# Kernel optimization log

Hardware: AMD Instinct MI355X
Metric: run time of the kernel (lower is better)

## Reference

```python
import jax, jax.numpy as jnp
import numpy as np


def setup_inputs() -> dict:
    key = jax.random.key(0)
    k1, k2 = jax.random.split(key)
    B, C, H, W = 64, 2048, 16, 16
    P = 200
    x = jax.random.normal(k1, (B, C, H, W), dtype=jnp.float32)
    prototype_vectors = jax.random.normal(k2, (P, C), dtype=jnp.float32)
    return {"x": x, "prototype_vectors": prototype_vectors}


def reference(x, prototype_vectors):
    # x: (B, C, H, W); prototypes: (P, C)
    B, C, H, W = x.shape
    P = prototype_vectors.shape[0]
    x_flat = x.reshape(B, C, H * W)                      # (B, C, S)
    # broadcasted (B,P,C,S) subtraction; same math, GEMM for cross term)
    x_sq = jnp.sum(x_flat * x_flat, axis=1)              # (B, S)
    p_sq = jnp.sum(prototype_vectors * prototype_vectors, axis=1)  # (P,)
    cross = jnp.einsum('pc,bcs->bps', prototype_vectors, x_flat)   # (B, P, S)
    distances = x_sq[:, None, :] + p_sq[None, :, None] - 2.0 * cross  # (B, P, S)
    similarities = -distances
    max_similarities = jnp.max(similarities, axis=2)     # (B, P)
    activation_maps = similarities.reshape(B, P, H, W)   # (B, P, H, W)
    return max_similarities, distances, activation_maps
```

## Files before the change

kernel.cpp:

```cpp
#include <hip/hip_runtime.h>

typedef float floatx4 __attribute__((ext_vector_type(4)));
typedef unsigned short ushortx4 __attribute__((ext_vector_type(4)));
typedef __bf16 bf16x8 __attribute__((ext_vector_type(8)));

#define B_ 64
#define C_ 2048
#define S_ 256
#define P_ 200
#define PM_ 256
#define ST_ 32
#define NST_ 8
#define NKT_ 32

__device__ __forceinline__ unsigned short f2bf(float f) {
  unsigned int u = __float_as_uint(f);
  u += 0x7FFFu + ((u >> 16) & 1u);
  return (unsigned short)(u >> 16);
}

__global__ void __launch_bounds__(256) prep_kernel(const float* __restrict__ proto,
                                                   unsigned short* __restrict__ wsp,
                                                   float* __restrict__ wpsq) {
  const int r = blockIdx.x;
  const int t = threadIdx.x;
  floatx4 v0 = {0.f,0.f,0.f,0.f}, v1 = {0.f,0.f,0.f,0.f};
  if (r < P_) {
    v0 = *reinterpret_cast<const floatx4*>(proto + (size_t)r * C_ + t * 8);
    v1 = *reinterpret_cast<const floatx4*>(proto + (size_t)r * C_ + t * 8 + 4);
  }
  float s = 0.f;
  ushortx4 h0, h1;
#pragma unroll
  for (int i = 0; i < 4; ++i) {
    s += v0[i]*v0[i] + v1[i]*v1[i];
    h0[i] = f2bf(v0[i]); h1[i] = f2bf(v1[i]);
  }
  const int u = (t >> 3) * 16384 + (r >> 4) * 1024 + (t & 7) * 128 + (r & 15) * 8;
  *reinterpret_cast<ushortx4*>(wsp + u) = h0;
  *reinterpret_cast<ushortx4*>(wsp + u + 4) = h1;

#pragma unroll
  for (int o = 32; o > 0; o >>= 1) s += __shfl_down(s, o);
  __shared__ float red[4];
  if ((t & 63) == 0) red[t >> 6] = s;
  __syncthreads();
  if (t == 0) wpsq[r] = red[0] + red[1] + red[2] + red[3];
}

__global__ void __launch_bounds__(512, 4) main_kernel(const float* __restrict__ x,
    const unsigned short* __restrict__ wsp, const float* __restrict__ wpsq,
    float* __restrict__ out_dist, float* __restrict__ out_act,
    float* __restrict__ wpmax) {
  __shared__ unsigned short lds[36864];

  const int t = threadIdx.x;
  const int lane = t & 63;
  const int w = t >> 6;
  const int lg = lane >> 4, l15 = lane & 15;
  const int b = blockIdx.x >> 3, st = blockIdx.x & 7;

  const int s_ = lane & 31;
  const int h_ = lane >> 5;
  const float* xb = x + (size_t)b * (C_ * S_) + (size_t)(w * 8 + h_ * 4) * S_ + st * ST_ + s_;

  const int slot_w = (s_ & 15) ^ ((s_ & 8) >> 1) ^ ((s_ >> 4) << 1);
  const int wr_base = 32768 + (s_ >> 4) * 1024 + w * 128 + slot_w * 8 + h_ * 4;
  const int slot_r0 = l15 ^ ((l15 & 8) >> 1);

  floatx4 acc[2][2] = {};
  float xsq_s = 0.f;

#pragma unroll
  for (int q = 0; q < 4; ++q) {
    __builtin_amdgcn_global_load_lds(
      (const __attribute__((address_space(1))) unsigned int*)(wsp + (q * 512 + t) * 8),
      (__attribute__((address_space(3))) unsigned int*)
        ((__attribute__((address_space(3))) unsigned short*)lds + (q * 512 + t) * 8),
      16, 0, 0);
  }
  {
    float xj[4]; ushortx4 hv;
#pragma unroll
    for (int j = 0; j < 4; ++j) xj[j] = xb[j * S_];
#pragma unroll
    for (int j = 0; j < 4; ++j) { xsq_s += xj[j] * xj[j]; hv[j] = f2bf(xj[j]); }
    *reinterpret_cast<ushortx4*>(&lds[wr_base]) = hv;
  }
  __syncthreads();

  for (int kt = 0; kt < NKT_; ++kt) {
    const int cur = kt & 1, nb = cur ^ 1;
    float xj[4];
    if (kt < NKT_ - 1) {
      const unsigned short* gsrc = wsp + (size_t)(kt + 1) * 16384;
#pragma unroll
      for (int q = 0; q < 4; ++q) {
        __builtin_amdgcn_global_load_lds(
          (const __attribute__((address_space(1))) unsigned int*)(gsrc + (q * 512 + t) * 8),
          (__attribute__((address_space(3))) unsigned int*)
            ((__attribute__((address_space(3))) unsigned short*)lds + nb * 16384 + (q * 512 + t) * 8),
          16, 0, 0);
      }
      const float* xsrc = xb + (size_t)(kt + 1) * 64 * S_;
#pragma unroll
      for (int j = 0; j < 4; ++j) xj[j] = xsrc[j * S_];
    }
    {
      const unsigned short* As_c = lds + cur * 16384;
      const unsigned short* Bs_c = lds + 32768 + cur * 2048;
#pragma unroll
      for (int ks = 0; ks < 2; ++ks) {
        const int ko = (ks * 4 + lg) * 128;
        const bf16x8 a0 = *reinterpret_cast<const bf16x8*>(As_c + (w * 2 + 0) * 1024 + ko + l15 * 8);
        const bf16x8 a1 = *reinterpret_cast<const bf16x8*>(As_c + (w * 2 + 1) * 1024 + ko + l15 * 8);
        const bf16x8 b0 = *reinterpret_cast<const bf16x8*>(Bs_c + ko + slot_r0 * 8);
        const bf16x8 b1 = *reinterpret_cast<const bf16x8*>(Bs_c + 1024 + ko + (slot_r0 ^ 2) * 8);
        acc[0][0] = __builtin_amdgcn_mfma_f32_16x16x32_bf16(a0, b0, acc[0][0], 0, 0, 0);
        acc[0][1] = __builtin_amdgcn_mfma_f32_16x16x32_bf16(a0, b1, acc[0][1], 0, 0, 0);
        acc[1][0] = __builtin_amdgcn_mfma_f32_16x16x32_bf16(a1, b0, acc[1][0], 0, 0, 0);
        acc[1][1] = __builtin_amdgcn_mfma_f32_16x16x32_bf16(a1, b1, acc[1][1], 0, 0, 0);
      }
    }
    if (kt < NKT_ - 1) {
      ushortx4 hv;
#pragma unroll
      for (int j = 0; j < 4; ++j) { xsq_s += xj[j] * xj[j]; hv[j] = f2bf(xj[j]); }
      *reinterpret_cast<ushortx4*>(&lds[wr_base + nb * 2048]) = hv;
    }
    __syncthreads();
  }

  float* xpart = reinterpret_cast<float*>(&lds[32768]);
  float* xsqf  = xpart + 256;
  {
    const float v = xsq_s + __shfl_xor(xsq_s, 32);
    if (lane < 32) xpart[w * 32 + lane] = v;
  }
  __syncthreads();
  if (t < 32) {
    float s2 = 0.f;
#pragma unroll
    for (int w2 = 0; w2 < 8; ++w2) s2 += xpart[w2 * 32 + t];
    xsqf[t] = s2;
  }
  __syncthreads();

  const float xn0 = xsqf[l15], xn1 = xsqf[16 + l15];
#pragma unroll
  for (int mi = 0; mi < 2; ++mi)
#pragma unroll
    for (int r = 0; r < 4; ++r) {
      const int m = w * 32 + mi * 16 + lg * 4 + r;
      const float ps = (m < P_) ? wpsq[m] : 0.f;
      const float d0 = xn0 + ps - 2.0f * acc[mi][0][r];
      const float d1 = xn1 + ps - 2.0f * acc[mi][1][r];
      if (m < P_) {
        const size_t gi = (size_t)(b * P_ + m) * S_ + st * ST_ + l15;
        out_dist[gi] = d0;       out_dist[gi + 16] = d1;
        out_act[gi]  = -d0;      out_act[gi + 16]  = -d1;
      }
      float rm = fmaxf(-d0, -d1);
#pragma unroll
      for (int off = 1; off < 16; off <<= 1) rm = fmaxf(rm, __shfl_xor(rm, off));
      if (l15 == 0 && m < P_) wpmax[(size_t)((b << 8) + m) * 8 + st] = rm;
    }
}

__global__ void __launch_bounds__(256) fin_kernel(const float* __restrict__ wpmax,
                                                  float* __restrict__ out_max) {
  const int i = blockIdx.x * 256 + threadIdx.x;
  if (i >= B_ * P_) return;
  const int b = i / P_;
  const int p = i - b * P_;
  const float* q = wpmax + (size_t)((b << 8) + p) * 8;
  const floatx4 v0 = *reinterpret_cast<const floatx4*>(q);
  const floatx4 v1 = *reinterpret_cast<const floatx4*>(q + 4);
  out_max[i] = fmaxf(fmaxf(fmaxf(v0[0], v0[1]), fmaxf(v0[2], v0[3])),
                     fmaxf(fmaxf(v1[0], v1[1]), fmaxf(v1[2], v1[3])));
}

extern "C" void kernel_launch(void* const* d_in, const int* in_sizes, int n_in,
                              void* d_out, int out_size, void* d_ws, size_t ws_size,
                              hipStream_t stream) {
  (void)in_sizes; (void)n_in; (void)out_size; (void)ws_size;
  const float* x = (const float*)d_in[0];
  const float* proto = (const float*)d_in[1];
  float* out = (float*)d_out;

  unsigned short* wsp = (unsigned short*)d_ws;
  float* wpsq  = (float*)((char*)d_ws + (size_t)NKT_ * 16384 * 2);
  float* wpmax = (float*)((char*)d_ws + (size_t)NKT_ * 16384 * 2 + 1024);

  float* out_max  = out;
  float* out_dist = out + B_ * P_;
  float* out_act  = out + B_ * P_ + B_ * P_ * S_;

  prep_kernel<<<PM_, 256, 0, stream>>>(proto, wsp, wpsq);
  main_kernel<<<B_ * NST_, 512, 0, stream>>>(x, wsp, wpsq, out_dist, out_act, wpmax);
  fin_kernel<<<(B_ * P_ + 255) / 256, 256, 0, stream>>>(wpmax, out_max);
}
```

Baseline: 223.1 us.

## Load prototype A-fragments directly into registers instead of staging through LDS

The bf16 prototype tile is no longer copied into shared memory with global_load_lds. Each wave now loads its own A fragments straight from global memory into registers, double-buffered across iterations, and only the x tile is staged in LDS. This shrinks LDS use from about 72KB to 8KB per block, which could allow higher occupancy and removes the A-tile LDS reads. The barrier is replaced by a manual lgkmcnt wait plus s_barrier, and the loop is unrolled by two so the register buffers can alternate. The cost is more VGPRs and per-wave global loads whose latency is now exposed to each wave.

```diff
diff --git a/kernel.cpp b/kernel.cpp
--- a/kernel.cpp
+++ b/kernel.cpp
@@ -1,6 +1,7 @@
 #include <hip/hip_runtime.h>
 
 typedef float floatx4 __attribute__((ext_vector_type(4)));
+typedef unsigned int uintx4 __attribute__((ext_vector_type(4)));
 typedef unsigned short ushortx4 __attribute__((ext_vector_type(4)));
 typedef __bf16 bf16x8 __attribute__((ext_vector_type(8)));
 
@@ -52,7 +53,7 @@
     const unsigned short* __restrict__ wsp, const float* __restrict__ wpsq,
     float* __restrict__ out_dist, float* __restrict__ out_act,
     float* __restrict__ wpmax) {
-  __shared__ unsigned short lds[36864];
+  __shared__ unsigned short lds[4096];
 
   const int t = threadIdx.x;
   const int lane = t & 63;
@@ -65,73 +66,71 @@
   const float* xb = x + (size_t)b * (C_ * S_) + (size_t)(w * 8 + h_ * 4) * S_ + st * ST_ + s_;
 
   const int slot_w = (s_ & 15) ^ ((s_ & 8) >> 1) ^ ((s_ >> 4) << 1);
-  const int wr_base = 32768 + (s_ >> 4) * 1024 + w * 128 + slot_w * 8 + h_ * 4;
+  const int wr_base = (s_ >> 4) * 1024 + w * 128 + slot_w * 8 + h_ * 4;
   const int slot_r0 = l15 ^ ((l15 & 8) >> 1);
+
+  const unsigned short* ap = wsp + w * 2048 + lg * 128 + l15 * 8;
 
   floatx4 acc[2][2] = {};
   float xsq_s = 0.f;
 
-#pragma unroll
-  for (int q = 0; q < 4; ++q) {
-    __builtin_amdgcn_global_load_lds(
-      (const __attribute__((address_space(1))) unsigned int*)(wsp + (q * 512 + t) * 8),
-      (__attribute__((address_space(3))) unsigned int*)
-        ((__attribute__((address_space(3))) unsigned short*)lds + (q * 512 + t) * 8),
-      16, 0, 0);
-  }
-  {
-    float xj[4]; ushortx4 hv;
-#pragma unroll
-    for (int j = 0; j < 4; ++j) xj[j] = xb[j * S_];
-#pragma unroll
-    for (int j = 0; j < 4; ++j) { xsq_s += xj[j] * xj[j]; hv[j] = f2bf(xj[j]); }
-    *reinterpret_cast<ushortx4*>(&lds[wr_base]) = hv;
-  }
-  __syncthreads();
-
-  for (int kt = 0; kt < NKT_; ++kt) {
-    const int cur = kt & 1, nb = cur ^ 1;
-    float xj[4];
-    if (kt < NKT_ - 1) {
-      const unsigned short* gsrc = wsp + (size_t)(kt + 1) * 16384;
-#pragma unroll
-      for (int q = 0; q < 4; ++q) {
-        __builtin_amdgcn_global_load_lds(
-          (const __attribute__((address_space(1))) unsigned int*)(gsrc + (q * 512 + t) * 8),
-          (__attribute__((address_space(3))) unsigned int*)
-            ((__attribute__((address_space(3))) unsigned short*)lds + nb * 16384 + (q * 512 + t) * 8),
-          16, 0, 0);
-      }
-      const float* xsrc = xb + (size_t)(kt + 1) * 64 * S_;
-#pragma unroll
-      for (int j = 0; j < 4; ++j) xj[j] = xsrc[j * S_];
+#define LOADA(dst, T) do { const unsigned short* pp = ap + (size_t)(T) * 16384; \
+    dst[0] = *reinterpret_cast<const uintx4*>(pp);        \
+    dst[1] = *reinterpret_cast<const uintx4*>(pp + 512);  \
+    dst[2] = *reinterpret_cast<const uintx4*>(pp + 1024); \
+    dst[3] = *reinterpret_cast<const uintx4*>(pp + 1536); } while (0)
+
+#define LOADX(xv, T) do { const float* xs = xb + (size_t)(T) * 64 * S_; \
+    xv[0] = xs[0]; xv[1] = xs[S_]; xv[2] = xs[2*S_]; xv[3] = xs[3*S_]; } while (0)
+
+#define STAGEB(buf, xv) do { ushortx4 hv;                                  \
+    _Pragma("unroll") for (int j = 0; j < 4; ++j) {                        \
+      xsq_s += xv[j] * xv[j]; hv[j] = f2bf(xv[j]); }                       \
+    *reinterpret_cast<ushortx4*>(&lds[(buf) * 2048 + wr_base]) = hv; } while (0)
+
+#define BARRIER() asm volatile("s_waitcnt lgkmcnt(0)\n\ts_barrier" ::: "memory")
+
+#define COMPUTE(A, buf) do { const unsigned short* Bs_c = lds + (buf) * 2048;          \
+    _Pragma("unroll") for (int ks = 0; ks < 2; ++ks) {                                  \
+      const int ko = (ks * 4 + lg) * 128;                                               \
+      const bf16x8 a0 = __builtin_bit_cast(bf16x8, A[ks]);                              \
+      const bf16x8 a1 = __builtin_bit_cast(bf16x8, A[2 + ks]);                          \
+      const bf16x8 b0 = *reinterpret_cast<const bf16x8*>(Bs_c + ko + slot_r0 * 8);      \
+      const bf16x8 b1 = *reinterpret_cast<const bf16x8*>(Bs_c + 1024 + ko + (slot_r0 ^ 2) * 8); \
+      acc[0][0] = __builtin_amdgcn_mfma_f32_16x16x32_bf16(a0, b0, acc[0][0], 0, 0, 0);  \
+      acc[0][1] = __builtin_amdgcn_mfma_f32_16x16x32_bf16(a0, b1, acc[0][1], 0, 0, 0);  \
+      acc[1][0] = __builtin_amdgcn_mfma_f32_16x16x32_bf16(a1, b0, acc[1][0], 0, 0, 0);  \
+      acc[1][1] = __builtin_amdgcn_mfma_f32_16x16x32_bf16(a1, b1, acc[1][1], 0, 0, 0);  \
+    } } while (0)
+
+  uintx4 aQ[4], aR[4];
+  float xj[4];
+  LOADX(xj, 0);
+  LOADA(aQ, 0);
+  STAGEB(0, xj);
+  BARRIER();
+
+  for (int kt = 0; kt < NKT_; kt += 2) {
+    float xn[4];
+    LOADX(xn, kt + 1);
+    LOADA(aR, kt + 1);
+    COMPUTE(aQ, 0);
+    STAGEB(1, xn);
+    BARRIER();
+    if (kt + 2 < NKT_) {
+      float xm[4];
+      LOADX(xm, kt + 2);
+      LOADA(aQ, kt + 2);
+      COMPUTE(aR, 1);
+      STAGEB(0, xm);
+      BARRIER();
+    } else {
+      COMPUTE(aR, 1);
     }
-    {
-      const unsigned short* As_c = lds + cur * 16384;
-      const unsigned short* Bs_c = lds + 32768 + cur * 2048;
-#pragma unroll
-      for (int ks = 0; ks < 2; ++ks) {
-        const int ko = (ks * 4 + lg) * 128;
-        const bf16x8 a0 = *reinterpret_cast<const bf16x8*>(As_c + (w * 2 + 0) * 1024 + ko + l15 * 8);
-        const bf16x8 a1 = *reinterpret_cast<const bf16x8*>(As_c + (w * 2 + 1) * 1024 + ko + l15 * 8);
-        const bf16x8 b0 = *reinterpret_cast<const bf16x8*>(Bs_c + ko + slot_r0 * 8);
-        const bf16x8 b1 = *reinterpret_cast<const bf16x8*>(Bs_c + 1024 + ko + (slot_r0 ^ 2) * 8);
-        acc[0][0] = __builtin_amdgcn_mfma_f32_16x16x32_bf16(a0, b0, acc[0][0], 0, 0, 0);
-        acc[0][1] = __builtin_amdgcn_mfma_f32_16x16x32_bf16(a0, b1, acc[0][1], 0, 0, 0);
-        acc[1][0] = __builtin_amdgcn_mfma_f32_16x16x32_bf16(a1, b0, acc[1][0], 0, 0, 0);
-        acc[1][1] = __builtin_amdgcn_mfma_f32_16x16x32_bf16(a1, b1, acc[1][1], 0, 0, 0);
-      }
-    }
-    if (kt < NKT_ - 1) {
-      ushortx4 hv;
-#pragma unroll
-      for (int j = 0; j < 4; ++j) { xsq_s += xj[j] * xj[j]; hv[j] = f2bf(xj[j]); }
-      *reinterpret_cast<ushortx4*>(&lds[wr_base + nb * 2048]) = hv;
-    }
-    __syncthreads();
-  }
-
-  float* xpart = reinterpret_cast<float*>(&lds[32768]);
+  }
+  __syncthreads();
+
+  float* xpart = reinterpret_cast<float*>(&lds[0]);
   float* xsqf  = xpart + 256;
   {
     const float v = xsq_s + __shfl_xor(xsq_s, 32);
```

After: 220.0 us. No clear change (-1.4%).
